# Performance work log

Hardware: AMD Instinct MI355X
Metric: run time of the kernel (lower is better)

## Reference

```python
import jax, jax.numpy as jnp
import numpy as np

B, H, W, C = 32, 64, 64, 256
WS, SS, NH = 8, 4, 8  # window size, shift size, num heads
HD = C // NH
N = WS * WS  # tokens per window
NW = (H // WS) * (W // WS)  # windows per image


def _rel_pos_index():
    coords = np.stack(np.meshgrid(np.arange(WS), np.arange(WS), indexing='ij'))  # [2,ws,ws]
    cf = coords.reshape(2, -1)
    rel = (cf[:, :, None] - cf[:, None, :]).transpose(1, 2, 0)  # [N,N,2]
    rel[:, :, 0] += WS - 1
    rel[:, :, 1] += WS - 1
    rel[:, :, 0] *= 2 * WS - 1
    return rel.sum(-1)  # [N,N] ints in [0,(2ws-1)^2)


def _shift_mask():
    # Standard Swin SW-MSA mask: -100 where tokens come from different regions.
    img = np.zeros((H, W))
    cnt = 0
    for hs in (slice(0, -WS), slice(-WS, -SS), slice(-SS, None)):
        for ws_ in (slice(0, -WS), slice(-WS, -SS), slice(-SS, None)):
            img[hs, ws_] = cnt
            cnt += 1
    mw = img.reshape(H // WS, WS, W // WS, WS).transpose(0, 2, 1, 3).reshape(-1, N)  # [nW,N]
    diff = mw[:, None, :] - mw[:, :, None]
    return np.where(diff != 0, -100.0, 0.0).astype(np.float32)  # [nW,N,N]


_RPI = _rel_pos_index()
_MASK = jnp.asarray(_shift_mask())


def _ln(x, g, b, eps=1e-5):
    m = jnp.mean(x, axis=-1, keepdims=True)
    v = jnp.var(x, axis=-1, keepdims=True)
    return (x - m) * jax.lax.rsqrt(v + eps) * g + b


def setup_inputs() -> dict:
    key = jax.random.key(0)
    ks = jax.random.split(key, 8)
    f = lambda k, shape: jax.random.normal(k, shape, jnp.float32) * 0.02
    return {
        'x': jax.random.normal(ks[0], (B, H * W, C), jnp.float32),
        'norm1_g': jnp.ones((C,), jnp.float32),
        'norm1_b': jnp.zeros((C,), jnp.float32),
        'qkv_w': f(ks[1], (3 * C, C)),
        'qkv_b': jnp.zeros((3 * C,), jnp.float32),
        'rpb_table': f(ks[2], ((2 * WS - 1) ** 2, NH)),
        'proj_w': f(ks[3], (C, C)),
        'proj_b': jnp.zeros((C,), jnp.float32),
        'norm2_g': jnp.ones((C,), jnp.float32),
        'norm2_b': jnp.zeros((C,), jnp.float32),
        'fc1_w': f(ks[4], (4 * C, C)),
        'fc1_b': jnp.zeros((4 * C,), jnp.float32),
        'fc2_w': f(ks[5], (C, 4 * C)),
        'fc2_b': jnp.zeros((C,), jnp.float32),
    }


def reference(x, norm1_g, norm1_b, qkv_w, qkv_b, rpb_table, proj_w, proj_b,
              norm2_g, norm2_b, fc1_w, fc1_b, fc2_w, fc2_b):
    shortcut = x
    h = _ln(x, norm1_g, norm1_b).reshape(B, H, W, C)
    # cyclic shift
    h = jnp.roll(h, shift=(-SS, -SS), axis=(1, 2))
    # window partition -> [B*nW, N, C]
    h = h.reshape(B, H // WS, WS, W // WS, WS, C)
    h = h.transpose(0, 1, 3, 2, 4, 5).reshape(B * NW, N, C)
    # windowed multi-head attention with relative position bias + shift mask
    qkv = (h @ qkv_w.T + qkv_b).reshape(B * NW, N, 3, NH, HD)
    q, k, v = qkv[:, :, 0], qkv[:, :, 1], qkv[:, :, 2]  # [Bn, N, NH, HD]
    scale = HD ** -0.5
    attn = jnp.einsum('bqhd,bkhd->bhqk', q * scale, k)  # [Bn, NH, N, N]
    bias = rpb_table[_RPI.reshape(-1)].reshape(N, N, NH).transpose(2, 0, 1)  # [NH,N,N]
    attn = attn + bias[None]
    attn = attn.reshape(B, NW, NH, N, N) + _MASK[None, :, None]
    attn = jax.nn.softmax(attn.reshape(B * NW, NH, N, N), axis=-1)
    h = jnp.einsum('bhqk,bkhd->bqhd', attn, v).reshape(B * NW, N, C)
    h = h @ proj_w.T + proj_b
    # window reverse
    h = h.reshape(B, H // WS, W // WS, WS, WS, C)
    h = h.transpose(0, 1, 3, 2, 4, 5).reshape(B, H, W, C)
    # reverse cyclic shift
    h = jnp.roll(h, shift=(SS, SS), axis=(1, 2)).reshape(B, H * W, C)
    x = shortcut + h  # drop_path = identity in eval
    # MLP
    m = _ln(x, norm2_g, norm2_b)
    m = jax.nn.gelu(m @ fc1_w.T + fc1_b)
    m = m @ fc2_w.T + fc2_b
    return x + m
```

## Files before the change

### kernel.cpp

```cpp
#include <hip/hip_runtime.h>
#include <hip/hip_bf16.h>
#include <stdint.h>

using f16 = _Float16;
typedef _Float16 f16x8 __attribute__((ext_vector_type(8)));
typedef float f32x4 __attribute__((ext_vector_type(4)));

static constexpr int HW = 4096;
static constexpr int CC = 256;
static constexpr int ROWS = 131072;
static constexpr int ACH = 4;
static constexpr int AROWS = ROWS / ACH;
static constexpr int CWINS = AROWS / 64;
static constexpr int SSH = 4;

static constexpr size_t OFF_WQ = 0;
static constexpr size_t OFF_WP = OFF_WQ + (size_t)768*256*2;
static constexpr size_t OFF_W1 = OFF_WP + (size_t)256*256*2;
static constexpr size_t OFF_W2 = OFF_W1 + (size_t)1024*256*2;
static constexpr size_t OFF_R1 = OFF_W2 + (size_t)256*1024*2;
static constexpr size_t OFF_R2 = OFF_R1 + (size_t)ROWS*CC*2;

__device__ __forceinline__ void gload16(void* lds, const void* g) {
    __builtin_amdgcn_global_load_lds(
        (const __attribute__((address_space(1))) unsigned int*)g,
        (__attribute__((address_space(3))) unsigned int*)lds, 16, 0, 0);
}

__global__ void k_cvt(const float* __restrict__ s, f16* __restrict__ d, int n) {
    int i = blockIdx.x * 256 + threadIdx.x;
    if (i < n) d[i] = (f16)s[i];
}

__global__ __launch_bounds__(256) void k_ln(const float* __restrict__ x,
                                            const float* __restrict__ g,
                                            const float* __restrict__ be,
                                            f16* __restrict__ dst, int rowbase) {
    int lrow = blockIdx.x * 4 + (threadIdx.x >> 6);
    int grow = rowbase + lrow;
    int lane = threadIdx.x & 63;
    int n = grow & 63, win = (grow >> 6) & 63, b = grow >> 12;
    int hh  = ((win >> 3) << 3) | (n >> 3);
    int wwc = ((win & 7) << 3) | (n & 7);
    int ho = (hh + SSH) & 63, wo = (wwc + SSH) & 63;
    size_t srow = (size_t)b * HW + ho * 64 + wo;
    float4 v = ((const float4*)(x + srow * CC))[lane];
    float s  = v.x + v.y + v.z + v.w;
    float s2 = v.x*v.x + v.y*v.y + v.z*v.z + v.w*v.w;
#pragma unroll
    for (int off = 32; off; off >>= 1) { s += __shfl_xor(s, off); s2 += __shfl_xor(s2, off); }
    float mean = s * (1.f/256.f);
    float rstd = rsqrtf(s2 * (1.f/256.f) - mean*mean + 1e-5f);
    float4 gv = ((const float4*)g)[lane];
    float4 bv = ((const float4*)be)[lane];
    f16 ob[4];
    ob[0] = (f16)((v.x-mean)*rstd*gv.x + bv.x);
    ob[1] = (f16)((v.y-mean)*rstd*gv.y + bv.y);
    ob[2] = (f16)((v.z-mean)*rstd*gv.z + bv.z);
    ob[3] = (f16)((v.w-mean)*rstd*gv.w + bv.w);
    *(uint2*)(dst + (size_t)lrow * CC + lane * 4) = *(const uint2*)ob;
}

__global__ __launch_bounds__(256) void k_qkv(const f16* __restrict__ A,
                                             const f16* __restrict__ Wt,
                                             const float* __restrict__ bias,
                                             f16* __restrict__ q, f16* __restrict__ kk,
                                             f16* __restrict__ vv) {
    __shared__ f16 As[2][128 * 32];
    __shared__ f16 Bs[2][128 * 32];
    const int tid = threadIdx.x;
    const int m0 = blockIdx.x * 128, n0 = blockIdx.y * 128;
    const int wave = tid >> 6, lane = tid & 63;
    const int wm = (wave >> 1) * 64, wn = (wave & 1) * 64;
    const int lr = lane & 15, kq = lane >> 4;
    const int i0 = wave * 128 + lane;
    const int r0 = i0 >> 2, c0 = (i0 & 3) * 8;
    const int i1 = i0 + 64;
    const int r1 = i1 >> 2, c1 = (i1 & 3) * 8;
    const int base0 = wave * 1024, base1 = base0 + 512;

    auto stage = [&](int b, int k0) {
        gload16(&As[b][base0], &A [(size_t)(m0 + r0) * CC + k0 + c0]);
        gload16(&Bs[b][base0], &Wt[(size_t)(n0 + r0) * CC + k0 + c0]);
        gload16(&As[b][base1], &A [(size_t)(m0 + r1) * CC + k0 + c1]);
        gload16(&Bs[b][base1], &Wt[(size_t)(n0 + r1) * CC + k0 + c1]);
    };

    f32x4 acc[4][4];
#pragma unroll
    for (int i = 0; i < 4; i++)
#pragma unroll
        for (int j = 0; j < 4; j++) acc[i][j] = f32x4{0.f, 0.f, 0.f, 0.f};

    stage(0, 0);
    __syncthreads();
    for (int s = 0; s < 8; s++) {
        int cur = s & 1;
        if (s + 1 < 8) stage(cur ^ 1, (s + 1) * 32);
        f16x8 af[4], bfv[4];
#pragma unroll
        for (int i = 0; i < 4; i++) {
            af[i]  = *(const f16x8*)(&As[cur][(wm + i * 16 + lr) * 32 + kq * 8]);
            bfv[i] = *(const f16x8*)(&Bs[cur][(wn + i * 16 + lr) * 32 + kq * 8]);
        }
#pragma unroll
        for (int mi = 0; mi < 4; mi++)
#pragma unroll
            for (int ni = 0; ni < 4; ni++)
                acc[mi][ni] = __builtin_amdgcn_mfma_f32_16x16x32_f16(af[mi], bfv[ni], acc[mi][ni], 0, 0, 0);
        __syncthreads();
    }

#pragma unroll
    for (int mi = 0; mi < 4; mi++)
#pragma unroll
        for (int ni = 0; ni < 4; ni++)
#pragma unroll
            for (int j = 0; j < 4; j++) {
                int lrow = m0 + wm + mi * 16 + kq * 4 + j;
                int gcol = n0 + wn + ni * 16 + lr;
                float val = acc[mi][ni][j] + bias[gcol];
                int s = gcol >> 8, h2 = (gcol >> 5) & 7, d = gcol & 31;
                if (s == 0) val *= 0.1767766952966369f;
                f16* dst = (s == 0) ? q : (s == 1 ? kk : vv);
                int winl = lrow >> 6, n = lrow & 63;
                dst[(((size_t)winl * 8 + h2) * 64 + n) * 32 + d] = (f16)val;
            }
}

__global__ __launch_bounds__(256, 2) void k_proj(const f16* __restrict__ A,
                                                 const f16* __restrict__ Wt,
                                                 const float* __restrict__ bias,
                                                 const float* __restrict__ x_in,
                                                 float* __restrict__ outf,
                                                 f16* __restrict__ m_out,
                                                 const float* __restrict__ g2,
                                                 const float* __restrict__ b2) {
    __shared__ f16 As[2][64 * 32];
    __shared__ f16 Bs[2][256 * 32];
    __shared__ float rsum[4][64];
    __shared__ float rsq[4][64];
    const int tid = threadIdx.x;
    const int m0 = blockIdx.x * 64;
    const int wave = tid >> 6, lane = tid & 63;
    const int lr = lane & 15, kq = lane >> 4;
    const int ar = tid >> 2, ac = (tid & 3) * 8;

    auto stage = [&](int b, int k0) {
        gload16(&As[b][wave * 512], &A[(size_t)(m0 + ar) * CC + k0 + ac]);
#pragma unroll
        for (int r = 0; r < 4; r++)
            gload16(&Bs[b][(r * 256 + wave * 64) * 8],
                    &Wt[(size_t)(r * 64 + ar) * CC + k0 + ac]);
    };

    f32x4 acc[4][4];
#pragma unroll
    for (int i = 0; i < 4; i++)
#pragma unroll
        for (int j = 0; j < 4; j++) acc[i][j] = f32x4{0.f, 0.f, 0.f, 0.f};

    stage(0, 0);
    __syncthreads();
    for (int s = 0; s < 8; s++) {
        int cur = s & 1;
        if (s + 1 < 8) stage(cur ^ 1, (s + 1) * 32);
        f16x8 af[4], bfv[4];
#pragma unroll
        for (int i = 0; i < 4; i++) {
            af[i]  = *(const f16x8*)(&As[cur][(i * 16 + lr) * 32 + kq * 8]);
            bfv[i] = *(const f16x8*)(&Bs[cur][(wave * 64 + i * 16 + lr) * 32 + kq * 8]);
        }
#pragma unroll
        for (int mi = 0; mi < 4; mi++)
#pragma unroll
            for (int ni = 0; ni < 4; ni++)
                acc[mi][ni] = __builtin_amdgcn_mfma_f32_16x16x32_f16(af[mi], bfv[ni], acc[mi][ni], 0, 0, 0);
        __syncthreads();
    }

    int srows[4][4];
#pragma unroll
    for (int mi = 0; mi < 4; mi++)
#pragma unroll
        for (int j = 0; j < 4; j++) {
            int row = m0 + mi * 16 + kq * 4 + j;
            int n = row & 63, win = (row >> 6) & 63, b = row >> 12;
            int hh  = ((win >> 3) << 3) | (n >> 3);
            int wwc = ((win & 7) << 3) | (n & 7);
            int ho = (hh + SSH) & 63, wo = (wwc + SSH) & 63;
            srows[mi][j] = b * HW + ho * 64 + wo;
        }
    float bv[4], gv[4], b2v[4];
#pragma unroll
    for (int ni = 0; ni < 4; ni++) {
        int gcol = wave * 64 + ni * 16 + lr;
        bv[ni] = bias[gcol]; gv[ni] = g2[gcol]; b2v[ni] = b2[gcol];
    }
    float ps[4][4], qs[4][4];
#pragma unroll
    for (int mi = 0; mi < 4; mi++)
#pragma unroll
        for (int j = 0; j < 4; j++) { ps[mi][j] = 0.f; qs[mi][j] = 0.f; }
#pragma unroll
    for (int mi = 0; mi < 4; mi++)
#pragma unroll
        for (int ni = 0; ni < 4; ni++) {
            int gcol = wave * 64 + ni * 16 + lr;
#pragma unroll
            for (int j = 0; j < 4; j++) {
                size_t idx = (size_t)srows[mi][j] * CC + gcol;
                float v = acc[mi][ni][j] + bv[ni] + x_in[idx];
                acc[mi][ni][j] = v;
                outf[idx] = v;
                ps[mi][j] += v; qs[mi][j] += v * v;
            }
        }
#pragma unroll
    for (int off = 1; off < 16; off <<= 1)
#pragma unroll
        for (int mi = 0; mi < 4; mi++)
#pragma unroll
            for (int j = 0; j < 4; j++) {
                ps[mi][j] += __shfl_xor(ps[mi][j], off);
                qs[mi][j] += __shfl_xor(qs[mi][j], off);
            }
    if (lr == 0) {
#pragma unroll
        for (int mi = 0; mi < 4; mi++)
#pragma unroll
            for (int j = 0; j < 4; j++) {
                int rl = mi * 16 + kq * 4 + j;
                rsum[wave][rl] = ps[mi][j];
                rsq[wave][rl]  = qs[mi][j];
            }
    }
    __syncthreads();
    float mean_a[4][4], rstd_a[4][4];
#pragma unroll
    for (int mi = 0; mi < 4; mi++)
#pragma unroll
        for (int j = 0; j < 4; j++) {
            int rl = mi * 16 + kq * 4 + j;
            float s  = rsum[0][rl] + rsum[1][rl] + rsum[2][rl] + rsum[3][rl];
            float s2 = rsq[0][rl] + rsq[1][rl] + rsq[2][rl] + rsq[3][rl];
            float mean = s * (1.f/256.f);
            float var  = s2 * (1.f/256.f) - mean * mean;
            mean_a[mi][j] = mean;
            rstd_a[mi][j] = rsqrtf(var + 1e-5f);
        }
#pragma unroll
    for (int mi = 0; mi < 4; mi++)
#pragma unroll
        for (int ni = 0; ni < 4; ni++) {
            int gcol = wave * 64 + ni * 16 + lr;
#pragma unroll
            for (int j = 0; j < 4; j++) {
                float m = (acc[mi][ni][j] - mean_a[mi][j]) * rstd_a[mi][j] * gv[ni] + b2v[ni];
                m_out[(size_t)srows[mi][j] * CC + gcol] = (f16)m;
            }
        }
}

__global__ __launch_bounds__(256) void k_mlp2(const f16* __restrict__ A,
                                              const f16* __restrict__ w1,
                                              const f16* __restrict__ w2,
                                              const float* __restrict__ fb1,
                                              const float* __restrict__ fb2,
                                              float* __restrict__ out) {
    __shared__ char sm[49152];
    char* hbuf = sm;
    char* S    = sm + 16384;
    f16* As  = (f16*)S;
    f16* Bs1 = (f16*)(S + 8192);
    f16* Bs2 = (f16*)S;
    const int tid = threadIdx.x, wave = tid >> 6, lane = tid & 63;
    const int lr = lane & 15, kq = lane >> 4;
    const int m0 = blockIdx.x * 64;
    const int ar = tid >> 2, ac = (tid & 3) * 8;

    f32x4 acc2[4][4];
#pragma unroll
    for (int i = 0; i < 4; i++)
#pragma unroll
        for (int j = 0; j < 4; j++) acc2[i][j] = f32x4{0.f, 0.f, 0.f, 0.f};

    for (int nb = 0; nb < 8; nb++) {
        auto stage1 = [&](int b, int k0) {
            gload16(&As[b * 2048 + wave * 512], &A[(size_t)(m0 + ar) * CC + k0 + ac]);
            gload16(&Bs1[b * 4096 + wave * 512],
                    &w1[(size_t)(nb * 128 + ar) * CC + k0 + ac]);
            gload16(&Bs1[b * 4096 + 2048 + wave * 512],
                    &w1[(size_t)(nb * 128 + 64 + ar) * CC + k0 + ac]);
        };
        f32x4 acc1[2][4];
#pragma unroll
        for (int i = 0; i < 2; i++)
#pragma unroll
            for (int j = 0; j < 4; j++) acc1[i][j] = f32x4{0.f, 0.f, 0.f, 0.f};
        stage1(0, 0);
        __syncthreads();
#pragma unroll
        for (int ks = 0; ks < 8; ks++) {
            int cur = ks & 1;
            if (ks + 1 < 8) stage1(cur ^ 1, (ks + 1) * 32);
            f16x8 aw1[2], bx[4];
#pragma unroll
            for (int hi = 0; hi < 2; hi++)
                aw1[hi] = *(const f16x8*)(&Bs1[cur * 4096 +
                                               (wave * 32 + hi * 16 + lr) * 32 + kq * 8]);
#pragma unroll
            for (int qi = 0; qi < 4; qi++)
                bx[qi] = *(const f16x8*)(&As[cur * 2048 + (qi * 16 + lr) * 32 + kq * 8]);
#pragma unroll
            for (int hi = 0; hi < 2; hi++)
#pragma unroll
                for (int qi = 0; qi < 4; qi++)
                    acc1[hi][qi] = __builtin_amdgcn_mfma_f32_16x16x32_f16(
                        aw1[hi], bx[qi], acc1[hi][qi], 0, 0, 0);
            __syncthreads();
        }
#pragma unroll
        for (int hi = 0; hi < 2; hi++) {
            float4 bb4 = *(const float4*)&fb1[nb * 128 + wave * 32 + hi * 16 + kq * 4];
            const float bb[4] = {bb4.x, bb4.y, bb4.z, bb4.w};
            const int hidb = wave * 64 + hi * 32 + kq * 8;
#pragma unroll
            for (int qi = 0; qi < 4; qi++) {
                f16 t4[4];
#pragma unroll
                for (int j = 0; j < 4; j++) {
                    float v = acc1[hi][qi][j] + bb[j];
                    float z = 0.7978845608028654f * (v + 0.044715f * v * v * v);
                    float t = 1.f - 2.f / (__expf(2.f * z) + 1.f);
                    t4[j] = (f16)(0.5f * v * (1.f + t));
                }
                int qrow = qi * 16 + lr;
                *(uint2*)(hbuf + qrow * 256 + (hidb ^ ((qrow & 7) << 4))) =
                    *(const uint2*)t4;
            }
        }
        auto stage2 = [&](int b, int k0) {
#pragma unroll
            for (int t = 0; t < 4; t++)
                gload16(&Bs2[b * 8192 + t * 2048 + wave * 512],
                        &w2[(size_t)(t * 64 + ar) * 1024 + nb * 128 + k0 + ac]);
        };
        stage2(0, 0);
        __syncthreads();
#pragma unroll
        for (int ks = 0; ks < 4; ks++) {
            int cur = ks & 1;
            if (ks + 1 < 4) stage2(cur ^ 1, (ks + 1) * 32);
            f16x8 ah[4], bw[4];
#pragma unroll
            for (int mi = 0; mi < 4; mi++) {
                int row = mi * 16 + lr;
                ah[mi] = *(const f16x8*)(hbuf + row * 256 +
                                         ((ks * 64 + kq * 16) ^ ((row & 7) << 4)));
            }
#pragma unroll
            for (int ni = 0; ni < 4; ni++)
                bw[ni] = *(const f16x8*)(&Bs2[cur * 8192 +
                                              (wave * 64 + ni * 16 + lr) * 32 + kq * 8]);
#pragma unroll
            for (int mi = 0; mi < 4; mi++)
#pragma unroll
                for (int ni = 0; ni < 4; ni++)
                    acc2[mi][ni] = __builtin_amdgcn_mfma_f32_16x16x32_f16(
                        ah[mi], bw[ni], acc2[mi][ni], 0, 0, 0);
            __syncthreads();
        }
    }

#pragma unroll
    for (int mi = 0; mi < 4; mi++)
#pragma unroll
        for (int ni = 0; ni < 4; ni++)
#pragma unroll
            for (int j = 0; j < 4; j++) {
                int qrow = m0 + mi * 16 + kq * 4 + j;
                int oc = wave * 64 + ni * 16 + lr;
                size_t idx = (size_t)qrow * CC + oc;
                out[idx] = out[idx] + acc2[mi][ni][j] + fb2[oc];
            }
}

__global__ __launch_bounds__(64) void k_attn(const f16* __restrict__ q,
                                             const f16* __restrict__ kk,
                                             const f16* __restrict__ vv,
                                             const float* __restrict__ rpb,
                                             f16* __restrict__ aw, int winbase) {
    __shared__ char sm[17408];
    float* rl = (float*)(sm + 16384);
    const int wl = blockIdx.x >> 3, h = blockIdx.x & 7;
    const int lane = threadIdx.x;
    const int lr = lane & 15, kq = lane >> 4;
    const size_t base = ((size_t)wl * 8 + h) * 2048;

    for (int i = lane; i < 225; i += 64) rl[i] = rpb[i * 8 + h];

    {
        f16 vr[32];
        const uint4* vs = (const uint4*)(vv + base + lane * 32);
#pragma unroll
        for (int c = 0; c < 4; c++) *(uint4*)&vr[c * 8] = vs[c];
#pragma unroll
        for (int d = 0; d < 32; d++)
            *(f16*)(sm + 8192 + d * 128 + ((lane * 2) ^ ((d & 7) << 4))) = vr[d];
    }

    f16x8 kf[4], qf[4];
#pragma unroll
    for (int t = 0; t < 4; t++) {
        kf[t] = *(const f16x8*)(kk + base + (size_t)(t * 16 + lr) * 32 + kq * 8);
        qf[t] = *(const f16x8*)(q  + base + (size_t)(t * 16 + lr) * 32 + kq * 8);
    }

    f32x4 st[4][4];
#pragma unroll
    for (int mi = 0; mi < 4; mi++)
#pragma unroll
        for (int ni = 0; ni < 4; ni++) st[mi][ni] = f32x4{0.f, 0.f, 0.f, 0.f};
#pragma unroll
    for (int mi = 0; mi < 4; mi++)
#pragma unroll
        for (int ni = 0; ni < 4; ni++)
            st[mi][ni] = __builtin_amdgcn_mfma_f32_16x16x32_f16(kf[mi], qf[ni], st[mi][ni], 0, 0, 0);

    __syncthreads();

    const int gwin = (winbase + wl) & 63;
    const int wh = gwin >> 3, ww = gwin & 7;
    int yq[4], xq[4], rq[4];
#pragma unroll
    for (int ni = 0; ni < 4; ni++) {
        int qq = ni * 16 + lr;
        yq[ni] = qq >> 3; xq[ni] = qq & 7;
        rq[ni] = ((wh < 7) ? 0 : ((yq[ni] < 4) ? 1 : 2)) * 3 +
                 ((ww < 7) ? 0 : ((xq[ni] < 4) ? 1 : 2));
    }
#pragma unroll
    for (int mi = 0; mi < 4; mi++)
#pragma unroll
        for (int j = 0; j < 4; j++) {
            int kt = mi * 16 + kq * 4 + j;
            int yk = kt >> 3, xk = kt & 7;
            int rk = ((wh < 7) ? 0 : ((yk < 4) ? 1 : 2)) * 3 +
                     ((ww < 7) ? 0 : ((xk < 4) ? 1 : 2));
#pragma unroll
            for (int ni = 0; ni < 4; ni++) {
                float b = rl[(yq[ni] - yk + 7) * 15 + (xq[ni] - xk + 7)];
                if (rq[ni] != rk) b -= 100.f;
                st[mi][ni][j] += b;
            }
        }

    float mx[4] = {-1e30f, -1e30f, -1e30f, -1e30f};
#pragma unroll
    for (int mi = 0; mi < 4; mi++)
#pragma unroll
        for (int ni = 0; ni < 4; ni++)
#pragma unroll
            for (int j = 0; j < 4; j++) mx[ni] = fmaxf(mx[ni], st[mi][ni][j]);
#pragma unroll
    for (int ni = 0; ni < 4; ni++) {
        mx[ni] = fmaxf(mx[ni], __shfl_xor(mx[ni], 16));
        mx[ni] = fmaxf(mx[ni], __shfl_xor(mx[ni], 32));
    }
    float sme[4] = {0.f, 0.f, 0.f, 0.f};
#pragma unroll
    for (int mi = 0; mi < 4; mi++)
#pragma unroll
        for (int ni = 0; ni < 4; ni++)
#pragma unroll
            for (int j = 0; j < 4; j++) {
                float e = __expf(st[mi][ni][j] - mx[ni]);
                st[mi][ni][j] = e;
                sme[ni] += e;
            }
#pragma unroll
    for (int ni = 0; ni < 4; ni++) {
        sme[ni] += __shfl_xor(sme[ni], 16);
        sme[ni] += __shfl_xor(sme[ni], 32);
    }
    float inv[4];
#pragma unroll
    for (int ni = 0; ni < 4; ni++) inv[ni] = 1.f / sme[ni];

#pragma unroll
    for (int mi = 0; mi < 4; mi++)
#pragma unroll
        for (int ni = 0; ni < 4; ni++) {
            f16 t4[4];
#pragma unroll
            for (int j = 0; j < 4; j++) t4[j] = (f16)st[mi][ni][j];
            int qq = ni * 16 + lr;
            *(uint2*)(sm + qq * 128 + ((mi * 32 + kq * 8) ^ ((qq & 7) << 4))) =
                *(const uint2*)t4;
        }
    __syncthreads();

    f32x4 oa[2][4];
#pragma unroll
    for (int mi2 = 0; mi2 < 2; mi2++)
#pragma unroll
        for (int ni = 0; ni < 4; ni++) oa[mi2][ni] = f32x4{0.f, 0.f, 0.f, 0.f};
#pragma unroll
    for (int ks = 0; ks < 2; ks++) {
        f16x8 va[2], pb[4];
#pragma unroll
        for (int mi2 = 0; mi2 < 2; mi2++) {
            int row = mi2 * 16 + lr;
            va[mi2] = *(const f16x8*)(sm + 8192 + row * 128 +
                                      ((ks * 64 + kq * 16) ^ ((row & 7) << 4)));
        }
#pragma unroll
        for (int ni = 0; ni < 4; ni++) {
            int qq = ni * 16 + lr;
            pb[ni] = *(const f16x8*)(sm + qq * 128 +
                                     ((ks * 64 + kq * 16) ^ ((qq & 7) << 4)));
        }
#pragma unroll
        for (int mi2 = 0; mi2 < 2; mi2++)
#pragma unroll
            for (int ni = 0; ni < 4; ni++)
                oa[mi2][ni] = __builtin_amdgcn_mfma_f32_16x16x32_f16(va[mi2], pb[ni], oa[mi2][ni], 0, 0, 0);
    }

#pragma unroll
    for (int mi2 = 0; mi2 < 2; mi2++)
#pragma unroll
        for (int ni = 0; ni < 4; ni++) {
            f16 t4[4];
#pragma unroll
            for (int j = 0; j < 4; j++) t4[j] = (f16)(oa[mi2][ni][j] * inv[ni]);
            int qq = ni * 16 + lr;
            *(uint2*)(sm + 12288 + qq * 64 + ((mi2 * 32 + kq * 8) ^ ((qq & 3) << 4))) =
                *(const uint2*)t4;
        }
    __syncthreads();

    f16* dst = aw + ((size_t)(wl * 64 + lane)) * CC + h * 32;
#pragma unroll
    for (int c = 0; c < 4; c++) {
        uint4 wv = *(const uint4*)(sm + 12288 + lane * 64 +
                                   ((c * 16) ^ ((lane & 3) << 4)));
        *(uint4*)(dst + c * 8) = wv;
    }
}

extern "C" void kernel_launch(void* const* d_in, const int* in_sizes, int n_in,
                              void* d_out, int out_size, void* d_ws, size_t ws_size,
                              hipStream_t stream) {
    (void)in_sizes; (void)n_in; (void)out_size; (void)ws_size;
    const float* x      = (const float*)d_in[0];
    const float* g1     = (const float*)d_in[1];
    const float* b1     = (const float*)d_in[2];
    const float* qkv_w  = (const float*)d_in[3];
    const float* qkv_b  = (const float*)d_in[4];
    const float* rpb    = (const float*)d_in[5];
    const float* proj_w = (const float*)d_in[6];
    const float* proj_b = (const float*)d_in[7];
    const float* g2     = (const float*)d_in[8];
    const float* b2     = (const float*)d_in[9];
    const float* fc1_w  = (const float*)d_in[10];
    const float* fc1_b  = (const float*)d_in[11];
    const float* fc2_w  = (const float*)d_in[12];
    const float* fc2_b  = (const float*)d_in[13];
    float* out = (float*)d_out;
    char* ws = (char*)d_ws;
    f16* wq = (f16*)(ws + OFF_WQ);
    f16* wp = (f16*)(ws + OFF_WP);
    f16* w1 = (f16*)(ws + OFF_W1);
    f16* w2 = (f16*)(ws + OFF_W2);
    f16* awb = (f16*)(ws + OFF_R1);
    static constexpr size_t QSZ = (size_t)CWINS * 8 * 64 * 32 * 2;
    f16* hwin = (f16*)(ws + OFF_R2);
    f16* qb   = (f16*)(ws + OFF_R2 + QSZ);
    f16* kb   = (f16*)(ws + OFF_R2 + 2 * QSZ);
    f16* vb   = (f16*)(ws + OFF_R2 + 3 * QSZ);
    f16* m_in = (f16*)(ws + OFF_R2);

    k_cvt<<<768, 256, 0, stream>>>(qkv_w, wq, 768 * 256);
    k_cvt<<<256, 256, 0, stream>>>(proj_w, wp, 256 * 256);
    k_cvt<<<1024, 256, 0, stream>>>(fc1_w, w1, 1024 * 256);
    k_cvt<<<1024, 256, 0, stream>>>(fc2_w, w2, 1024 * 256);

    for (int c = 0; c < ACH; c++) {
        k_ln<<<AROWS / 4, 256, 0, stream>>>(x, g1, b1, hwin, c * AROWS);
        k_qkv<<<dim3(AROWS / 128, 6), 256, 0, stream>>>(
            hwin, wq, qkv_b, qb, kb, vb);
        k_attn<<<CWINS * 8, 64, 0, stream>>>(
            qb, kb, vb, rpb, awb + (size_t)c * AROWS * CC, c * CWINS);
    }
    k_proj<<<ROWS / 64, 256, 0, stream>>>(awb, wp, proj_b, x, out, m_in, g2, b2);

    k_mlp2<<<ROWS / 64, 256, 0, stream>>>(m_in, w1, w2, fc1_b, fc2_b, out);
}
```

Baseline: 626.9 us.

## Store GEMM LDS tiles in MFMA fragment order to avoid bank conflicts

Changes how the qkv, proj and MLP GEMM kernels stage their operand tiles into shared memory. Each 16-row chunk is now written in the exact per-lane order the MFMA fragment reads, so every lane reads a contiguous 16 bytes (lane*8). This is meant to remove LDS bank conflicts from the strided row-major reads. The MLP hidden buffer gets the same fragment-ordered layout in place of the XOR swizzle. The tanh-GELU is also rewritten in a cheaper sigmoid form, v*rcp(1+exp(...)), which uses an approximate reciprocal and so changes rounding slightly.

```diff
diff --git a/kernel.cpp b/kernel.cpp
--- a/kernel.cpp
+++ b/kernel.cpp
@@ -73,17 +73,15 @@
     const int wave = tid >> 6, lane = tid & 63;
     const int wm = (wave >> 1) * 64, wn = (wave & 1) * 64;
     const int lr = lane & 15, kq = lane >> 4;
-    const int i0 = wave * 128 + lane;
-    const int r0 = i0 >> 2, c0 = (i0 & 3) * 8;
-    const int i1 = i0 + 64;
-    const int r1 = i1 >> 2, c1 = (i1 & 3) * 8;
-    const int base0 = wave * 1024, base1 = base0 + 512;
 
     auto stage = [&](int b, int k0) {
-        gload16(&As[b][base0], &A [(size_t)(m0 + r0) * CC + k0 + c0]);
-        gload16(&Bs[b][base0], &Wt[(size_t)(n0 + r0) * CC + k0 + c0]);
-        gload16(&As[b][base1], &A [(size_t)(m0 + r1) * CC + k0 + c1]);
-        gload16(&Bs[b][base1], &Wt[(size_t)(n0 + r1) * CC + k0 + c1]);
+#pragma unroll
+        for (int t = 0; t < 2; t++) {
+            int c = wave * 2 + t;
+            int row = c * 16 + lr;
+            gload16(&As[b][c * 512], &A [(size_t)(m0 + row) * CC + k0 + kq * 8]);
+            gload16(&Bs[b][c * 512], &Wt[(size_t)(n0 + row) * CC + k0 + kq * 8]);
+        }
     };
 
     f32x4 acc[4][4];
@@ -100,8 +98,8 @@
         f16x8 af[4], bfv[4];
 #pragma unroll
         for (int i = 0; i < 4; i++) {
-            af[i]  = *(const f16x8*)(&As[cur][(wm + i * 16 + lr) * 32 + kq * 8]);
-            bfv[i] = *(const f16x8*)(&Bs[cur][(wn + i * 16 + lr) * 32 + kq * 8]);
+            af[i]  = *(const f16x8*)(&As[cur][((wave >> 1) * 4 + i) * 512 + lane * 8]);
+            bfv[i] = *(const f16x8*)(&Bs[cur][((wave & 1) * 4 + i) * 512 + lane * 8]);
         }
 #pragma unroll
         for (int mi = 0; mi < 4; mi++)
@@ -144,14 +142,14 @@
     const int m0 = blockIdx.x * 64;
     const int wave = tid >> 6, lane = tid & 63;
     const int lr = lane & 15, kq = lane >> 4;
-    const int ar = tid >> 2, ac = (tid & 3) * 8;
 
     auto stage = [&](int b, int k0) {
-        gload16(&As[b][wave * 512], &A[(size_t)(m0 + ar) * CC + k0 + ac]);
-#pragma unroll
-        for (int r = 0; r < 4; r++)
-            gload16(&Bs[b][(r * 256 + wave * 64) * 8],
-                    &Wt[(size_t)(r * 64 + ar) * CC + k0 + ac]);
+        gload16(&As[b][wave * 512], &A[(size_t)(m0 + wave * 16 + lr) * CC + k0 + kq * 8]);
+#pragma unroll
+        for (int r = 0; r < 4; r++) {
+            int c = wave * 4 + r;
+            gload16(&Bs[b][c * 512], &Wt[(size_t)(c * 16 + lr) * CC + k0 + kq * 8]);
+        }
     };
 
     f32x4 acc[4][4];
@@ -168,8 +166,8 @@
         f16x8 af[4], bfv[4];
 #pragma unroll
         for (int i = 0; i < 4; i++) {
-            af[i]  = *(const f16x8*)(&As[cur][(i * 16 + lr) * 32 + kq * 8]);
-            bfv[i] = *(const f16x8*)(&Bs[cur][(wave * 64 + i * 16 + lr) * 32 + kq * 8]);
+            af[i]  = *(const f16x8*)(&As[cur][i * 512 + lane * 8]);
+            bfv[i] = *(const f16x8*)(&Bs[cur][(wave * 4 + i) * 512 + lane * 8]);
         }
 #pragma unroll
         for (int mi = 0; mi < 4; mi++)
@@ -277,7 +275,6 @@
     const int tid = threadIdx.x, wave = tid >> 6, lane = tid & 63;
     const int lr = lane & 15, kq = lane >> 4;
     const int m0 = blockIdx.x * 64;
-    const int ar = tid >> 2, ac = (tid & 3) * 8;
 
     f32x4 acc2[4][4];
 #pragma unroll
@@ -287,11 +284,14 @@
 
     for (int nb = 0; nb < 8; nb++) {
         auto stage1 = [&](int b, int k0) {
-            gload16(&As[b * 2048 + wave * 512], &A[(size_t)(m0 + ar) * CC + k0 + ac]);
-            gload16(&Bs1[b * 4096 + wave * 512],
-                    &w1[(size_t)(nb * 128 + ar) * CC + k0 + ac]);
-            gload16(&Bs1[b * 4096 + 2048 + wave * 512],
-                    &w1[(size_t)(nb * 128 + 64 + ar) * CC + k0 + ac]);
+            gload16(&As[b * 2048 + wave * 512],
+                    &A[(size_t)(m0 + wave * 16 + lr) * CC + k0 + kq * 8]);
+#pragma unroll
+            for (int t = 0; t < 2; t++) {
+                int c = wave * 2 + t;
+                gload16(&Bs1[b * 4096 + c * 512],
+                        &w1[(size_t)(nb * 128 + c * 16 + lr) * CC + k0 + kq * 8]);
+            }
         };
         f32x4 acc1[2][4];
 #pragma unroll
@@ -307,11 +307,10 @@
             f16x8 aw1[2], bx[4];
 #pragma unroll
             for (int hi = 0; hi < 2; hi++)
-                aw1[hi] = *(const f16x8*)(&Bs1[cur * 4096 +
-                                               (wave * 32 + hi * 16 + lr) * 32 + kq * 8]);
+                aw1[hi] = *(const f16x8*)(&Bs1[cur * 4096 + (wave * 2 + hi) * 512 + lane * 8]);
 #pragma unroll
             for (int qi = 0; qi < 4; qi++)
-                bx[qi] = *(const f16x8*)(&As[cur * 2048 + (qi * 16 + lr) * 32 + kq * 8]);
+                bx[qi] = *(const f16x8*)(&As[cur * 2048 + qi * 512 + lane * 8]);
 #pragma unroll
             for (int hi = 0; hi < 2; hi++)
 #pragma unroll
@@ -324,27 +323,26 @@
         for (int hi = 0; hi < 2; hi++) {
             float4 bb4 = *(const float4*)&fb1[nb * 128 + wave * 32 + hi * 16 + kq * 4];
             const float bb[4] = {bb4.x, bb4.y, bb4.z, bb4.w};
-            const int hidb = wave * 64 + hi * 32 + kq * 8;
+            const int dbase = wave * 4096 + (hi * 2 + (kq >> 1)) * 256 + lr * 16 + (kq & 1) * 8;
 #pragma unroll
             for (int qi = 0; qi < 4; qi++) {
                 f16 t4[4];
 #pragma unroll
                 for (int j = 0; j < 4; j++) {
                     float v = acc1[hi][qi][j] + bb[j];
-                    float z = 0.7978845608028654f * (v + 0.044715f * v * v * v);
-                    float t = 1.f - 2.f / (__expf(2.f * z) + 1.f);
-                    t4[j] = (f16)(0.5f * v * (1.f + t));
+                    float e = __expf(v * (-1.5957691216f - 0.07135482f * v * v));
+                    t4[j] = (f16)(v * __builtin_amdgcn_rcpf(1.f + e));
                 }
-                int qrow = qi * 16 + lr;
-                *(uint2*)(hbuf + qrow * 256 + (hidb ^ ((qrow & 7) << 4))) =
-                    *(const uint2*)t4;
+                *(uint2*)(hbuf + dbase + qi * 1024) = *(const uint2*)t4;
             }
         }
         auto stage2 = [&](int b, int k0) {
 #pragma unroll
-            for (int t = 0; t < 4; t++)
-                gload16(&Bs2[b * 8192 + t * 2048 + wave * 512],
-                        &w2[(size_t)(t * 64 + ar) * 1024 + nb * 128 + k0 + ac]);
+            for (int t = 0; t < 4; t++) {
+                int c = wave * 4 + t;
+                gload16(&Bs2[b * 8192 + c * 512],
+                        &w2[(size_t)(c * 16 + lr) * 1024 + nb * 128 + k0 + kq * 8]);
+            }
         };
         stage2(0, 0);
         __syncthreads();
@@ -354,15 +352,11 @@
             if (ks + 1 < 4) stage2(cur ^ 1, (ks + 1) * 32);
             f16x8 ah[4], bw[4];
 #pragma unroll
-            for (int mi = 0; mi < 4; mi++) {
-                int row = mi * 16 + lr;
-                ah[mi] = *(const f16x8*)(hbuf + row * 256 +
-                                         ((ks * 64 + kq * 16) ^ ((row & 7) << 4)));
-            }
+            for (int mi = 0; mi < 4; mi++)
+                ah[mi] = *(const f16x8*)(hbuf + ks * 4096 + mi * 1024 + lane * 16);
 #pragma unroll
             for (int ni = 0; ni < 4; ni++)
-                bw[ni] = *(const f16x8*)(&Bs2[cur * 8192 +
-                                              (wave * 64 + ni * 16 + lr) * 32 + kq * 8]);
+                bw[ni] = *(const f16x8*)(&Bs2[cur * 8192 + (wave * 4 + ni) * 512 + lane * 8]);
 #pragma unroll
             for (int mi = 0; mi < 4; mi++)
 #pragma unroll
```

Measured after the change: 735.3 us. +17.3%, slower.
